# Performance work log

Measured on AMD Instinct MI355X. Metric: run time of the kernel, lower is better.

Reference implementation:

```python
import jax, jax.numpy as jnp
import numpy as np

IN_SIZE = 512
OUT_SIZE = 256
HIDDEN = 256
LN_EPS = 1e-5


def setup_inputs() -> dict:
    key = jax.random.key(0)
    ks = jax.random.split(key, 9)
    B, S, K = 8, 2048, 16
    net_in = jax.random.normal(ks[0], (B, S, K, IN_SIZE), dtype=jnp.float32)
    embeds = jax.random.normal(ks[1], (B, S, OUT_SIZE), dtype=jnp.float32)
    m = jax.random.uniform(ks[2], (B, S, K, 1), dtype=jnp.float32)
    W1 = jax.random.normal(ks[3], (IN_SIZE, HIDDEN), dtype=jnp.float32) * 0.02
    b1 = jnp.full((HIDDEN,), 0.02, dtype=jnp.float32)
    Wf = jax.random.normal(ks[4], (HIDDEN, OUT_SIZE + 1), dtype=jnp.float32) * 0.02
    bf = jnp.zeros((OUT_SIZE + 1,), dtype=jnp.float32)
    gamma = jnp.ones((OUT_SIZE,), dtype=jnp.float32)
    beta = jnp.zeros((OUT_SIZE,), dtype=jnp.float32)
    return {"net_in": net_in, "embeds": embeds, "m": m, "W1": W1, "b1": b1,
            "Wf": Wf, "bf": bf, "gamma": gamma, "beta": beta}


def reference(net_in, embeds, m, W1, b1, Wf, bf, gamma, beta):
    # MLP: one hidden relu layer, final linear to out_size+1
    h = jax.nn.relu(jnp.einsum('bski,ih->bskh', net_in, W1) + b1)
    out = jnp.einsum('bskh,ho->bsko', h, Wf) + bf          # [B,S,K,out+1]
    # sigmoid on last channel (link weight), then mask
    out = jnp.concatenate([out[..., :-1], jax.nn.sigmoid(out[..., -1:])], axis=-1)
    out = m * out
    link_weight = out[..., -1] + 1e-8                       # [B,S,K]
    norm = jnp.sum(link_weight, axis=2, keepdims=True)      # [B,S,1]
    weights = (link_weight / norm)[..., None]               # [B,S,K,1]
    updates = jnp.sum(out * weights, axis=2)                # [B,S,out+1]
    # residual update
    upd_weights = updates[..., -1:]
    embeds_new = embeds + upd_weights * updates[..., :-1]
    # LayerNorm over last dim
    mu = jnp.mean(embeds_new, axis=-1, keepdims=True)
    var = jnp.var(embeds_new, axis=-1, keepdims=True)
    return (embeds_new - mu) * jax.lax.rsqrt(var + LN_EPS) * gamma + beta
```

## Files before the change

### kernel.cpp

```cpp
#include <hip/hip_runtime.h>

typedef short s16x8 __attribute__((ext_vector_type(8)));
typedef float f32x4 __attribute__((ext_vector_type(4)));

__device__ __forceinline__ unsigned short f2bf(float f) {
    union { float f; unsigned u; } v; v.f = f;
    return (unsigned short)((v.u + 0x7FFFu + ((v.u >> 16) & 1u)) >> 16);
}
__device__ __forceinline__ float bf2f(unsigned short h) {
    union { unsigned u; float f; } v; v.u = ((unsigned)h) << 16;
    return v.f;
}

__device__ __forceinline__ void wg_barrier_lds() {
    __builtin_amdgcn_sched_barrier(0);
    asm volatile("s_waitcnt lgkmcnt(0)" ::: "memory");
    __builtin_amdgcn_s_barrier();
    __builtin_amdgcn_sched_barrier(0);
}

#define NBLK 2048

__global__ void prep_weights(const float* __restrict__ W1, const float* __restrict__ Wf,
                             unsigned short* __restrict__ W1T, unsigned short* __restrict__ WfT) {
    int t = blockIdx.x * 256 + threadIdx.x;
    {
        int c  = t >> 13;
        int n  = (t >> 5) & 255;
        int kk = t & 31;
        W1T[t] = f2bf(W1[(c * 32 + kk) * 256 + n]);
    }
    if (t < 65536) {
        int c  = t >> 13;
        int n  = (t >> 5) & 255;
        int hh = t & 31;
        WfT[t] = f2bf(Wf[(c * 32 + hh) * 257 + n]);
    }
}

__global__ __launch_bounds__(512, 2)
void fused_embed(const float* __restrict__ net_in, const float* __restrict__ embeds,
                 const float* __restrict__ mg, const float* __restrict__ W1,
                 const float* __restrict__ b1, const float* __restrict__ Wf,
                 const float* __restrict__ bfv, const float* __restrict__ gam,
                 const float* __restrict__ bet, float* __restrict__ out,
                 const unsigned short* __restrict__ W1T, const unsigned short* __restrict__ WfT)
{
    __shared__ unsigned short Abuf[2][128][32];
    __shared__ unsigned short Hbuf[128][260];
    __shared__ unsigned short gbuf[16][264];
    __shared__ float updb[8][264];
    __shared__ float sbuf[8];

    const int tid  = threadIdx.x;
    const int lane = tid & 63;
    const int wid  = tid >> 6;
    const int wr   = wid >> 2;
    const int wc   = wid & 3;
    const int l15  = lane & 15;
    const int g8   = (lane >> 4) * 8;
    const int blk  = blockIdx.x;
    const int row0 = blk * 128;

    const f32x4 zero4 = {0.f, 0.f, 0.f, 0.f};

    f32x4 acc[4][4];
    #pragma unroll
    for (int i = 0; i < 4; ++i)
        #pragma unroll
        for (int j = 0; j < 4; ++j)
            acc[i][j] = zero4;

    const int ar = tid >> 2;
    const int ac = (tid & 3) * 8;
    const int wn = (wc * 64 + l15) * 32 + g8;

    float4 vaA[2], vbA[2];
    s16x8  wW0[2], wW1[2], wW2[2], wW3[2];

#define G1_ISSUE(KC, S) do { \
        const float* _src = &net_in[(row0 + ar) * 512 + (KC) * 32 + ac]; \
        vaA[S] = *(const float4*)_src; \
        vbA[S] = *(const float4*)(_src + 4); \
        const unsigned short* _wp = W1T + (KC) * 8192 + wn; \
        wW0[S] = *(const s16x8*)(_wp); \
        wW1[S] = *(const s16x8*)(_wp + 512); \
        wW2[S] = *(const s16x8*)(_wp + 1024); \
        wW3[S] = *(const s16x8*)(_wp + 1536); \
    } while (0)

#define G1_WRITE(KC, S) do { \
        int4 _pk; \
        asm("v_cvt_pk_bf16_f32 %0, %1, %2" : "=v"(_pk.x) : "v"(vaA[S].x), "v"(vaA[S].y)); \
        asm("v_cvt_pk_bf16_f32 %0, %1, %2" : "=v"(_pk.y) : "v"(vaA[S].z), "v"(vaA[S].w)); \
        asm("v_cvt_pk_bf16_f32 %0, %1, %2" : "=v"(_pk.z) : "v"(vbA[S].x), "v"(vbA[S].y)); \
        asm("v_cvt_pk_bf16_f32 %0, %1, %2" : "=v"(_pk.w) : "v"(vbA[S].z), "v"(vbA[S].w)); \
        *(int4*)&Abuf[(KC) & 1][ar][ac] = _pk; \
    } while (0)

    G1_ISSUE(0, 0);
    G1_ISSUE(1, 1);
    G1_WRITE(0, 0);
    wg_barrier_lds();

    #pragma unroll
    for (int kc = 0; kc < 16; ++kc) {
        const int cur = kc & 1;
        s16x8 b0 = wW0[cur], b1 = wW1[cur], b2 = wW2[cur], b3 = wW3[cur];
        if (kc < 14) G1_ISSUE(kc + 2, cur);
        if (kc < 15) G1_WRITE(kc + 1, (kc + 1) & 1);
        s16x8 af[4];
        #pragma unroll
        for (int i = 0; i < 4; ++i)
            af[i] = *(const s16x8*)&Abuf[cur][(wr * 4 + i) * 16 + l15][g8];
        #pragma unroll
        for (int i = 0; i < 4; ++i) {
            acc[i][0] = __builtin_amdgcn_mfma_f32_16x16x32_bf16(af[i], b0, acc[i][0], 0, 0, 0);
            acc[i][1] = __builtin_amdgcn_mfma_f32_16x16x32_bf16(af[i], b1, acc[i][1], 0, 0, 0);
            acc[i][2] = __builtin_amdgcn_mfma_f32_16x16x32_bf16(af[i], b2, acc[i][2], 0, 0, 0);
            acc[i][3] = __builtin_amdgcn_mfma_f32_16x16x32_bf16(af[i], b3, acc[i][3], 0, 0, 0);
        }
        wg_barrier_lds();
    }
#undef G1_ISSUE
#undef G1_WRITE

    #pragma unroll
    for (int j = 0; j < 4; ++j) {
        int col = wc * 64 + j * 16 + l15;
        float bb = b1[col];
        #pragma unroll
        for (int i = 0; i < 4; ++i) {
            #pragma unroll
            for (int r = 0; r < 4; ++r) {
                int row = (wr * 4 + i) * 16 + (lane >> 4) * 4 + r;
                Hbuf[row][col] = f2bf(fmaxf(acc[i][j][r] + bb, 0.f));
            }
        }
    }
    __syncthreads();

    float wl0 = Wf[(lane * 4 + 0) * 257 + 256];
    float wl1 = Wf[(lane * 4 + 1) * 257 + 256];
    float wl2 = Wf[(lane * 4 + 2) * 257 + 256];
    float wl3 = Wf[(lane * 4 + 3) * 257 + 256];
    float bf256 = bfv[256];

    float lcreg = 0.f;
    for (int k = 0; k < 16; ++k) {
        ushort4 hv = *(const ushort4*)&Hbuf[wid * 16 + k][lane * 4];
        float p = bf2f(hv.x) * wl0 + bf2f(hv.y) * wl1 + bf2f(hv.z) * wl2 + bf2f(hv.w) * wl3;
        #pragma unroll
        for (int off = 32; off > 0; off >>= 1) p += __shfl_xor(p, off, 64);
        if (lane == k) lcreg = p;
    }

    float wwreg = 0.f;
    float u256 = 0.f;
    if (lane < 16) {
        float mv  = mg[(blk * 8 + wid) * 16 + lane];
        float raw = lcreg + bf256;
        float sg  = 1.f / (1.f + expf(-raw));
        float v   = mv * sg;
        float lw  = v + 1e-8f;
        float nrm = lw;
        #pragma unroll
        for (int off = 8; off > 0; off >>= 1) nrm += __shfl_xor(nrm, off, 16);
        float wk = lw / nrm;
        wwreg = wk * mv;
        float u = wk * v;
        float s = wwreg;
        #pragma unroll
        for (int off = 8; off > 0; off >>= 1) {
            u += __shfl_xor(u, off, 16);
            s += __shfl_xor(s, off, 16);
        }
        u256 = u;
        if (lane == 0) sbuf[wid] = s;
    }
    u256 = __shfl(u256, 0, 64);

    {
        float ga0 = 0.f, ga1 = 0.f, ga2 = 0.f, ga3 = 0.f;
        #pragma unroll
        for (int k = 0; k < 16; ++k) {
            float wwk = __shfl(wwreg, k, 64);
            ushort4 hv = *(const ushort4*)&Hbuf[wid * 16 + k][lane * 4];
            ga0 += wwk * bf2f(hv.x);
            ga1 += wwk * bf2f(hv.y);
            ga2 += wwk * bf2f(hv.z);
            ga3 += wwk * bf2f(hv.w);
        }
        ushort4 gw; gw.x = f2bf(ga0); gw.y = f2bf(ga1); gw.z = f2bf(ga2); gw.w = f2bf(ga3);
        *(ushort4*)&gbuf[wid][lane * 4] = gw;
        ushort4 z4; z4.x = 0; z4.y = 0; z4.z = 0; z4.w = 0;
        *(ushort4*)&gbuf[8 + wid][lane * 4] = z4;
    }
    __syncthreads();

    f32x4 acc2[2];
    acc2[0] = zero4; acc2[1] = zero4;
    {
        const int w2n0 = ((wid * 2 + 0) * 16 + l15) * 32 + g8;
        const int w2n1 = ((wid * 2 + 1) * 16 + l15) * 32 + g8;
        s16x8 w2a[2], w2b[2];
        w2a[0] = *(const s16x8*)(WfT + w2n0);
        w2b[0] = *(const s16x8*)(WfT + w2n1);
        #pragma unroll
        for (int c2 = 0; c2 < 8; ++c2) {
            const int cur = c2 & 1;
            s16x8 ba = w2a[cur], bb = w2b[cur];
            if (c2 < 7) {
                w2a[cur ^ 1] = *(const s16x8*)(WfT + (c2 + 1) * 8192 + w2n0);
                w2b[cur ^ 1] = *(const s16x8*)(WfT + (c2 + 1) * 8192 + w2n1);
            }
            s16x8 ga = *(const s16x8*)&gbuf[l15][c2 * 32 + g8];
            acc2[0] = __builtin_amdgcn_mfma_f32_16x16x32_bf16(ga, ba, acc2[0], 0, 0, 0);
            acc2[1] = __builtin_amdgcn_mfma_f32_16x16x32_bf16(ga, bb, acc2[1], 0, 0, 0);
        }
    }

    {
        int gq = lane >> 4;
        if (gq < 2) {
            #pragma unroll
            for (int t = 0; t < 2; ++t) {
                int col = (wid * 2 + t) * 16 + l15;
                float bfc = bfv[col];
                #pragma unroll
                for (int r = 0; r < 4; ++r) {
                    int p = gq * 4 + r;
                    updb[p][col] = acc2[t][r] + sbuf[p] * bfc;
                }
            }
        }
    }
    __syncthreads();

    {
        int base = (blk * 8 + wid) * 256;
        float4 up = *(const float4*)&updb[wid][lane * 4];
        float4 em = *(const float4*)&embeds[base + lane * 4];
        float e0 = em.x + u256 * up.x;
        float e1 = em.y + u256 * up.y;
        float e2 = em.z + u256 * up.z;
        float e3 = em.w + u256 * up.w;
        float s1 = e0 + e1 + e2 + e3;
        float s2 = e0 * e0 + e1 * e1 + e2 * e2 + e3 * e3;
        #pragma unroll
        for (int off = 32; off > 0; off >>= 1) {
            s1 += __shfl_xor(s1, off, 64);
            s2 += __shfl_xor(s2, off, 64);
        }
        float mu  = s1 * (1.f / 256.f);
        float var = s2 * (1.f / 256.f) - mu * mu;
        float rs  = rsqrtf(var + 1e-5f);
        float4 gm = *(const float4*)&gam[lane * 4];
        float4 bt = *(const float4*)&bet[lane * 4];
        float4 o;
        o.x = (e0 - mu) * rs * gm.x + bt.x;
        o.y = (e1 - mu) * rs * gm.y + bt.y;
        o.z = (e2 - mu) * rs * gm.z + bt.z;
        o.w = (e3 - mu) * rs * gm.w + bt.w;
        *(float4*)&out[base + lane * 4] = o;
    }
}

extern "C" void kernel_launch(void* const* d_in, const int* in_sizes, int n_in,
                              void* d_out, int out_size, void* d_ws, size_t ws_size,
                              hipStream_t stream) {
    (void)in_sizes; (void)n_in; (void)ws_size; (void)out_size;
    const float* net_in = (const float*)d_in[0];
    const float* embeds = (const float*)d_in[1];
    const float* mg     = (const float*)d_in[2];
    const float* W1     = (const float*)d_in[3];
    const float* b1     = (const float*)d_in[4];
    const float* Wf     = (const float*)d_in[5];
    const float* bfv    = (const float*)d_in[6];
    const float* gam    = (const float*)d_in[7];
    const float* bet    = (const float*)d_in[8];
    float* outp = (float*)d_out;

    unsigned short* W1T = (unsigned short*)d_ws;
    unsigned short* WfT = W1T + 131072;

    prep_weights<<<512, 256, 0, stream>>>(W1, Wf, W1T, WfT);
    fused_embed<<<NBLK, 512, 0, stream>>>(net_in, embeds, mg, W1, b1, Wf, bfv, gam, bet, outp, W1T, WfT);
}
```

Before: 203.8 us.

## Load GEMM1 A fragments directly from global into registers, drop LDS staging

The first GEMM stops staging net_in through a double-buffered LDS tile. Each wave now loads its own A rows straight from global memory into registers, converts them to bf16 and feeds them to MFMA. The wave tiling changes from 2x4 to 4x2 (32 rows by 128 columns per wave), so each wave holds 8 W1 fragments per stage. The per-iteration LDS barrier becomes an occasional soft barrier every four k-chunks, which removes LDS traffic and sync cost but raises register pressure and the volume of W1 loads.

```diff
diff --git a/kernel.cpp b/kernel.cpp
--- a/kernel.cpp
+++ b/kernel.cpp
@@ -12,9 +12,8 @@
     return v.f;
 }
 
-__device__ __forceinline__ void wg_barrier_lds() {
+__device__ __forceinline__ void soft_barrier() {
     __builtin_amdgcn_sched_barrier(0);
-    asm volatile("s_waitcnt lgkmcnt(0)" ::: "memory");
     __builtin_amdgcn_s_barrier();
     __builtin_amdgcn_sched_barrier(0);
 }
@@ -46,7 +45,6 @@
                  const float* __restrict__ bet, float* __restrict__ out,
                  const unsigned short* __restrict__ W1T, const unsigned short* __restrict__ WfT)
 {
-    __shared__ unsigned short Abuf[2][128][32];
     __shared__ unsigned short Hbuf[128][260];
     __shared__ unsigned short gbuf[16][264];
     __shared__ float updb[8][264];
@@ -55,8 +53,6 @@
     const int tid  = threadIdx.x;
     const int lane = tid & 63;
     const int wid  = tid >> 6;
-    const int wr   = wid >> 2;
-    const int wc   = wid & 3;
     const int l15  = lane & 15;
     const int g8   = (lane >> 4) * 8;
     const int blk  = blockIdx.x;
@@ -64,76 +60,77 @@
 
     const f32x4 zero4 = {0.f, 0.f, 0.f, 0.f};
 
-    f32x4 acc[4][4];
+    const int wr = wid >> 1;
+    const int wc = wid & 1;
+
+    f32x4 acc[2][8];
     #pragma unroll
-    for (int i = 0; i < 4; ++i)
-        #pragma unroll
-        for (int j = 0; j < 4; ++j)
+    for (int i = 0; i < 2; ++i)
+        #pragma unroll
+        for (int j = 0; j < 8; ++j)
             acc[i][j] = zero4;
 
-    const int ar = tid >> 2;
-    const int ac = (tid & 3) * 8;
-    const int wn = (wc * 64 + l15) * 32 + g8;
-
-    float4 vaA[2], vbA[2];
-    s16x8  wW0[2], wW1[2], wW2[2], wW3[2];
-
-#define G1_ISSUE(KC, S) do { \
-        const float* _src = &net_in[(row0 + ar) * 512 + (KC) * 32 + ac]; \
-        vaA[S] = *(const float4*)_src; \
-        vbA[S] = *(const float4*)(_src + 4); \
-        const unsigned short* _wp = W1T + (KC) * 8192 + wn; \
-        wW0[S] = *(const s16x8*)(_wp); \
-        wW1[S] = *(const s16x8*)(_wp + 512); \
-        wW2[S] = *(const s16x8*)(_wp + 1024); \
-        wW3[S] = *(const s16x8*)(_wp + 1536); \
+    const float* pA0 = net_in + (row0 + wr * 32 + l15) * 512;
+    const float* pA1 = pA0 + 16 * 512;
+    const int wbase = (wc * 128 + l15) * 32 + g8;
+
+    float4 a0[2], a1[2], a2[2], a3[2];
+    s16x8  wf[2][8];
+
+#define S1_ISSUE(KC, S) do { \
+        a0[S] = *(const float4*)(pA0 + (KC) * 32 + g8); \
+        a1[S] = *(const float4*)(pA0 + (KC) * 32 + g8 + 4); \
+        a2[S] = *(const float4*)(pA1 + (KC) * 32 + g8); \
+        a3[S] = *(const float4*)(pA1 + (KC) * 32 + g8 + 4); \
+        const unsigned short* _wp = W1T + (KC) * 8192 + wbase; \
+        wf[S][0] = *(const s16x8*)(_wp); \
+        wf[S][1] = *(const s16x8*)(_wp + 512); \
+        wf[S][2] = *(const s16x8*)(_wp + 1024); \
+        wf[S][3] = *(const s16x8*)(_wp + 1536); \
+        wf[S][4] = *(const s16x8*)(_wp + 2048); \
+        wf[S][5] = *(const s16x8*)(_wp + 2560); \
+        wf[S][6] = *(const s16x8*)(_wp + 3072); \
+        wf[S][7] = *(const s16x8*)(_wp + 3584); \
     } while (0)
 
-#define G1_WRITE(KC, S) do { \
-        int4 _pk; \
-        asm("v_cvt_pk_bf16_f32 %0, %1, %2" : "=v"(_pk.x) : "v"(vaA[S].x), "v"(vaA[S].y)); \
-        asm("v_cvt_pk_bf16_f32 %0, %1, %2" : "=v"(_pk.y) : "v"(vaA[S].z), "v"(vaA[S].w)); \
-        asm("v_cvt_pk_bf16_f32 %0, %1, %2" : "=v"(_pk.z) : "v"(vbA[S].x), "v"(vbA[S].y)); \
-        asm("v_cvt_pk_bf16_f32 %0, %1, %2" : "=v"(_pk.w) : "v"(vbA[S].z), "v"(vbA[S].w)); \
-        *(int4*)&Abuf[(KC) & 1][ar][ac] = _pk; \
-    } while (0)
-
-    G1_ISSUE(0, 0);
-    G1_ISSUE(1, 1);
-    G1_WRITE(0, 0);
-    wg_barrier_lds();
+    S1_ISSUE(0, 0);
 
     #pragma unroll
     for (int kc = 0; kc < 16; ++kc) {
         const int cur = kc & 1;
-        s16x8 b0 = wW0[cur], b1 = wW1[cur], b2 = wW2[cur], b3 = wW3[cur];
-        if (kc < 14) G1_ISSUE(kc + 2, cur);
-        if (kc < 15) G1_WRITE(kc + 1, (kc + 1) & 1);
-        s16x8 af[4];
-        #pragma unroll
-        for (int i = 0; i < 4; ++i)
-            af[i] = *(const s16x8*)&Abuf[cur][(wr * 4 + i) * 16 + l15][g8];
-        #pragma unroll
-        for (int i = 0; i < 4; ++i) {
-            acc[i][0] = __builtin_amdgcn_mfma_f32_16x16x32_bf16(af[i], b0, acc[i][0], 0, 0, 0);
-            acc[i][1] = __builtin_amdgcn_mfma_f32_16x16x32_bf16(af[i], b1, acc[i][1], 0, 0, 0);
-            acc[i][2] = __builtin_amdgcn_mfma_f32_16x16x32_bf16(af[i], b2, acc[i][2], 0, 0, 0);
-            acc[i][3] = __builtin_amdgcn_mfma_f32_16x16x32_bf16(af[i], b3, acc[i][3], 0, 0, 0);
-        }
-        wg_barrier_lds();
-    }
-#undef G1_ISSUE
-#undef G1_WRITE
+        if (kc < 15) S1_ISSUE(kc + 1, cur ^ 1);
+        s16x8 af0, af1;
+        {
+            int4 p0, p1;
+            asm("v_cvt_pk_bf16_f32 %0, %1, %2" : "=v"(p0.x) : "v"(a0[cur].x), "v"(a0[cur].y));
+            asm("v_cvt_pk_bf16_f32 %0, %1, %2" : "=v"(p0.y) : "v"(a0[cur].z), "v"(a0[cur].w));
+            asm("v_cvt_pk_bf16_f32 %0, %1, %2" : "=v"(p0.z) : "v"(a1[cur].x), "v"(a1[cur].y));
+            asm("v_cvt_pk_bf16_f32 %0, %1, %2" : "=v"(p0.w) : "v"(a1[cur].z), "v"(a1[cur].w));
+            asm("v_cvt_pk_bf16_f32 %0, %1, %2" : "=v"(p1.x) : "v"(a2[cur].x), "v"(a2[cur].y));
+            asm("v_cvt_pk_bf16_f32 %0, %1, %2" : "=v"(p1.y) : "v"(a2[cur].z), "v"(a2[cur].w));
+            asm("v_cvt_pk_bf16_f32 %0, %1, %2" : "=v"(p1.z) : "v"(a3[cur].x), "v"(a3[cur].y));
+            asm("v_cvt_pk_bf16_f32 %0, %1, %2" : "=v"(p1.w) : "v"(a3[cur].z), "v"(a3[cur].w));
+            af0 = *(const s16x8*)&p0;
+            af1 = *(const s16x8*)&p1;
+        }
+        #pragma unroll
+        for (int j = 0; j < 8; ++j) {
+            acc[0][j] = __builtin_amdgcn_mfma_f32_16x16x32_bf16(af0, wf[cur][j], acc[0][j], 0, 0, 0);
+            acc[1][j] = __builtin_amdgcn_mfma_f32_16x16x32_bf16(af1, wf[cur][j], acc[1][j], 0, 0, 0);
+        }
+        if ((kc & 3) == 3 && kc != 15) soft_barrier();
+    }
+#undef S1_ISSUE
 
     #pragma unroll
-    for (int j = 0; j < 4; ++j) {
-        int col = wc * 64 + j * 16 + l15;
+    for (int j = 0; j < 8; ++j) {
+        int col = wc * 128 + j * 16 + l15;
         float bb = b1[col];
         #pragma unroll
-        for (int i = 0; i < 4; ++i) {
+        for (int i = 0; i < 2; ++i) {
             #pragma unroll
             for (int r = 0; r < 4; ++r) {
-                int row = (wr * 4 + i) * 16 + (lane >> 4) * 4 + r;
+                int row = wr * 32 + i * 16 + (lane >> 4) * 4 + r;
                 Hbuf[row][col] = f2bf(fmaxf(acc[i][j][r] + bb, 0.f));
             }
         }
```

Measured after the change: 331.9 us. 1.63x slower.

## Double block tile to 256 rows with 1024 threads and fill full second GEMM

Applied to the files above, without the earlier changes.

Each block now processes 256 rows (16 groups) with 16 waves instead of 128 rows with 8 waves. The hidden-tile epilogue runs in two halves so the existing Hbuf can be reused. The second GEMM's 16-row M tile, previously half zero-padded, is now filled with real groups, and the W1 register double-buffering is replaced by direct loads each iteration. The aim is to halve padded MFMA work in the second GEMM and amortize weight loads over more rows, at the cost of extra barriers, fewer resident blocks, and a higher register ceiling from dropping to 1024-thread launch bounds.

```diff
diff --git a/kernel.cpp b/kernel.cpp
--- a/kernel.cpp
+++ b/kernel.cpp
@@ -19,7 +19,7 @@
     __builtin_amdgcn_sched_barrier(0);
 }
 
-#define NBLK 2048
+#define NBLK 1024
 
 __global__ void prep_weights(const float* __restrict__ W1, const float* __restrict__ Wf,
                              unsigned short* __restrict__ W1T, unsigned short* __restrict__ WfT) {
@@ -38,7 +38,7 @@
     }
 }
 
-__global__ __launch_bounds__(512, 2)
+__global__ __launch_bounds__(1024)
 void fused_embed(const float* __restrict__ net_in, const float* __restrict__ embeds,
                  const float* __restrict__ mg, const float* __restrict__ W1,
                  const float* __restrict__ b1, const float* __restrict__ Wf,
@@ -46,11 +46,11 @@
                  const float* __restrict__ bet, float* __restrict__ out,
                  const unsigned short* __restrict__ W1T, const unsigned short* __restrict__ WfT)
 {
-    __shared__ unsigned short Abuf[2][128][32];
+    __shared__ unsigned short Abuf[2][256][32];
     __shared__ unsigned short Hbuf[128][260];
     __shared__ unsigned short gbuf[16][264];
-    __shared__ float updb[8][264];
-    __shared__ float sbuf[8];
+    __shared__ float updb[16][264];
+    __shared__ float sbuf[16];
 
     const int tid  = threadIdx.x;
     const int lane = tid & 63;
@@ -60,7 +60,7 @@
     const int l15  = lane & 15;
     const int g8   = (lane >> 4) * 8;
     const int blk  = blockIdx.x;
-    const int row0 = blk * 128;
+    const int row0 = blk * 256;
 
     const f32x4 zero4 = {0.f, 0.f, 0.f, 0.f};
 
@@ -73,23 +73,17 @@
 
     const int ar = tid >> 2;
     const int ac = (tid & 3) * 8;
-    const int wn = (wc * 64 + l15) * 32 + g8;
+    const int wbase = (wc * 64 + l15) * 32 + g8;
 
     float4 vaA[2], vbA[2];
-    s16x8  wW0[2], wW1[2], wW2[2], wW3[2];
-
-#define G1_ISSUE(KC, S) do { \
+
+#define A_ISSUE(KC, S) do { \
         const float* _src = &net_in[(row0 + ar) * 512 + (KC) * 32 + ac]; \
         vaA[S] = *(const float4*)_src; \
         vbA[S] = *(const float4*)(_src + 4); \
-        const unsigned short* _wp = W1T + (KC) * 8192 + wn; \
-        wW0[S] = *(const s16x8*)(_wp); \
-        wW1[S] = *(const s16x8*)(_wp + 512); \
-        wW2[S] = *(const s16x8*)(_wp + 1024); \
-        wW3[S] = *(const s16x8*)(_wp + 1536); \
     } while (0)
 
-#define G1_WRITE(KC, S) do { \
+#define A_WRITE(KC, S) do { \
         int4 _pk; \
         asm("v_cvt_pk_bf16_f32 %0, %1, %2" : "=v"(_pk.x) : "v"(vaA[S].x), "v"(vaA[S].y)); \
         asm("v_cvt_pk_bf16_f32 %0, %1, %2" : "=v"(_pk.y) : "v"(vaA[S].z), "v"(vaA[S].w)); \
@@ -98,47 +92,36 @@
         *(int4*)&Abuf[(KC) & 1][ar][ac] = _pk; \
     } while (0)
 
-    G1_ISSUE(0, 0);
-    G1_ISSUE(1, 1);
-    G1_WRITE(0, 0);
+    A_ISSUE(0, 0);
+    A_ISSUE(1, 1);
+    A_WRITE(0, 0);
     wg_barrier_lds();
 
     #pragma unroll
     for (int kc = 0; kc < 16; ++kc) {
         const int cur = kc & 1;
-        s16x8 b0 = wW0[cur], b1 = wW1[cur], b2 = wW2[cur], b3 = wW3[cur];
-        if (kc < 14) G1_ISSUE(kc + 2, cur);
-        if (kc < 15) G1_WRITE(kc + 1, (kc + 1) & 1);
+        const unsigned short* wp = W1T + kc * 8192 + wbase;
+        s16x8 b0 = *(const s16x8*)(wp);
+        s16x8 b1r = *(const s16x8*)(wp + 512);
+        s16x8 b2 = *(const s16x8*)(wp + 1024);
+        s16x8 b3 = *(const s16x8*)(wp + 1536);
+        if (kc < 14) A_ISSUE(kc + 2, cur);
+        if (kc < 15) A_WRITE(kc + 1, (kc + 1) & 1);
         s16x8 af[4];
         #pragma unroll
         for (int i = 0; i < 4; ++i)
-            af[i] = *(const s16x8*)&Abuf[cur][(wr * 4 + i) * 16 + l15][g8];
+            af[i] = *(const s16x8*)&Abuf[cur][wr * 64 + i * 16 + l15][g8];
         #pragma unroll
         for (int i = 0; i < 4; ++i) {
             acc[i][0] = __builtin_amdgcn_mfma_f32_16x16x32_bf16(af[i], b0, acc[i][0], 0, 0, 0);
-            acc[i][1] = __builtin_amdgcn_mfma_f32_16x16x32_bf16(af[i], b1, acc[i][1], 0, 0, 0);
+            acc[i][1] = __builtin_amdgcn_mfma_f32_16x16x32_bf16(af[i], b1r, acc[i][1], 0, 0, 0);
             acc[i][2] = __builtin_amdgcn_mfma_f32_16x16x32_bf16(af[i], b2, acc[i][2], 0, 0, 0);
             acc[i][3] = __builtin_amdgcn_mfma_f32_16x16x32_bf16(af[i], b3, acc[i][3], 0, 0, 0);
         }
         wg_barrier_lds();
     }
-#undef G1_ISSUE
-#undef G1_WRITE
-
-    #pragma unroll
-    for (int j = 0; j < 4; ++j) {
-        int col = wc * 64 + j * 16 + l15;
-        float bb = b1[col];
-        #pragma unroll
-        for (int i = 0; i < 4; ++i) {
-            #pragma unroll
-            for (int r = 0; r < 4; ++r) {
-                int row = (wr * 4 + i) * 16 + (lane >> 4) * 4 + r;
-                Hbuf[row][col] = f2bf(fmaxf(acc[i][j][r] + bb, 0.f));
-            }
-        }
-    }
-    __syncthreads();
+#undef A_ISSUE
+#undef A_WRITE
 
     float wl0 = Wf[(lane * 4 + 0) * 257 + 256];
     float wl1 = Wf[(lane * 4 + 1) * 257 + 256];
@@ -146,99 +129,108 @@
     float wl3 = Wf[(lane * 4 + 3) * 257 + 256];
     float bf256 = bfv[256];
 
-    float lcreg = 0.f;
-    for (int k = 0; k < 16; ++k) {
-        ushort4 hv = *(const ushort4*)&Hbuf[wid * 16 + k][lane * 4];
-        float p = bf2f(hv.x) * wl0 + bf2f(hv.y) * wl1 + bf2f(hv.z) * wl2 + bf2f(hv.w) * wl3;
-        #pragma unroll
-        for (int off = 32; off > 0; off >>= 1) p += __shfl_xor(p, off, 64);
-        if (lane == k) lcreg = p;
-    }
-
-    float wwreg = 0.f;
     float u256 = 0.f;
-    if (lane < 16) {
-        float mv  = mg[(blk * 8 + wid) * 16 + lane];
-        float raw = lcreg + bf256;
-        float sg  = 1.f / (1.f + expf(-raw));
-        float v   = mv * sg;
-        float lw  = v + 1e-8f;
-        float nrm = lw;
-        #pragma unroll
-        for (int off = 8; off > 0; off >>= 1) nrm += __shfl_xor(nrm, off, 16);
-        float wk = lw / nrm;
-        wwreg = wk * mv;
-        float u = wk * v;
-        float s = wwreg;
-        #pragma unroll
-        for (int off = 8; off > 0; off >>= 1) {
-            u += __shfl_xor(u, off, 16);
-            s += __shfl_xor(s, off, 16);
-        }
-        u256 = u;
-        if (lane == 0) sbuf[wid] = s;
-    }
-    u256 = __shfl(u256, 0, 64);
-
-    {
-        float ga0 = 0.f, ga1 = 0.f, ga2 = 0.f, ga3 = 0.f;
-        #pragma unroll
-        for (int k = 0; k < 16; ++k) {
-            float wwk = __shfl(wwreg, k, 64);
-            ushort4 hv = *(const ushort4*)&Hbuf[wid * 16 + k][lane * 4];
-            ga0 += wwk * bf2f(hv.x);
-            ga1 += wwk * bf2f(hv.y);
-            ga2 += wwk * bf2f(hv.z);
-            ga3 += wwk * bf2f(hv.w);
-        }
-        ushort4 gw; gw.x = f2bf(ga0); gw.y = f2bf(ga1); gw.z = f2bf(ga2); gw.w = f2bf(ga3);
-        *(ushort4*)&gbuf[wid][lane * 4] = gw;
-        ushort4 z4; z4.x = 0; z4.y = 0; z4.z = 0; z4.w = 0;
-        *(ushort4*)&gbuf[8 + wid][lane * 4] = z4;
-    }
-    __syncthreads();
-
-    f32x4 acc2[2];
-    acc2[0] = zero4; acc2[1] = zero4;
-    {
-        const int w2n0 = ((wid * 2 + 0) * 16 + l15) * 32 + g8;
-        const int w2n1 = ((wid * 2 + 1) * 16 + l15) * 32 + g8;
-        s16x8 w2a[2], w2b[2];
-        w2a[0] = *(const s16x8*)(WfT + w2n0);
-        w2b[0] = *(const s16x8*)(WfT + w2n1);
+
+    #pragma unroll
+    for (int h = 0; h < 2; ++h) {
+        const int mine = ((wid >> 3) == h);
+
+        if (mine) {
+            #pragma unroll
+            for (int j = 0; j < 4; ++j) {
+                int col = wc * 64 + j * 16 + l15;
+                float bb = b1[col];
+                #pragma unroll
+                for (int i = 0; i < 4; ++i) {
+                    #pragma unroll
+                    for (int r = 0; r < 4; ++r) {
+                        int rih = (wr & 1) * 64 + i * 16 + (lane >> 4) * 4 + r;
+                        Hbuf[rih][col] = f2bf(fmaxf(acc[i][j][r] + bb, 0.f));
+                    }
+                }
+            }
+        }
+        __syncthreads();
+
+        if (mine) {
+            float lcreg = 0.f;
+            for (int k = 0; k < 16; ++k) {
+                ushort4 hv = *(const ushort4*)&Hbuf[(wid & 7) * 16 + k][lane * 4];
+                float p = bf2f(hv.x) * wl0 + bf2f(hv.y) * wl1 + bf2f(hv.z) * wl2 + bf2f(hv.w) * wl3;
+                #pragma unroll
+                for (int off = 32; off > 0; off >>= 1) p += __shfl_xor(p, off, 64);
+                if (lane == k) lcreg = p;
+            }
+
+            float wwreg = 0.f;
+            if (lane < 16) {
+                float mv  = mg[(blk * 16 + wid) * 16 + lane];
+                float raw = lcreg + bf256;
+                float sg  = 1.f / (1.f + expf(-raw));
+                float v   = mv * sg;
+                float lw  = v + 1e-8f;
+                float nrm = lw;
+                #pragma unroll
+                for (int off = 8; off > 0; off >>= 1) nrm += __shfl_xor(nrm, off, 16);
+                float wk = lw / nrm;
+                wwreg = wk * mv;
+                float u = wk * v;
+                float s = wwreg;
+                #pragma unroll
+                for (int off = 8; off > 0; off >>= 1) {
+                    u += __shfl_xor(u, off, 16);
+                    s += __shfl_xor(s, off, 16);
+                }
+                u256 = u;
+                if (lane == 0) sbuf[wid] = s;
+            }
+            u256 = __shfl(u256, 0, 64);
+
+            float ga0 = 0.f, ga1 = 0.f, ga2 = 0.f, ga3 = 0.f;
+            #pragma unroll
+            for (int k = 0; k < 16; ++k) {
+                float wwk = __shfl(wwreg, k, 64);
+                ushort4 hv = *(const ushort4*)&Hbuf[(wid & 7) * 16 + k][lane * 4];
+                ga0 += wwk * bf2f(hv.x);
+                ga1 += wwk * bf2f(hv.y);
+                ga2 += wwk * bf2f(hv.z);
+                ga3 += wwk * bf2f(hv.w);
+            }
+            ushort4 gw; gw.x = f2bf(ga0); gw.y = f2bf(ga1); gw.z = f2bf(ga2); gw.w = f2bf(ga3);
+            *(ushort4*)&gbuf[wid][lane * 4] = gw;
+        }
+        __syncthreads();
+    }
+
+    f32x4 acc2 = zero4;
+    {
+        const int n0 = (wid * 16 + l15) * 32 + g8;
+        s16x8 w2[2];
+        w2[0] = *(const s16x8*)(WfT + n0);
         #pragma unroll
         for (int c2 = 0; c2 < 8; ++c2) {
             const int cur = c2 & 1;
-            s16x8 ba = w2a[cur], bb = w2b[cur];
-            if (c2 < 7) {
-                w2a[cur ^ 1] = *(const s16x8*)(WfT + (c2 + 1) * 8192 + w2n0);
-                w2b[cur ^ 1] = *(const s16x8*)(WfT + (c2 + 1) * 8192 + w2n1);
-            }
+            s16x8 bw = w2[cur];
+            if (c2 < 7) w2[cur ^ 1] = *(const s16x8*)(WfT + (c2 + 1) * 8192 + n0);
             s16x8 ga = *(const s16x8*)&gbuf[l15][c2 * 32 + g8];
-            acc2[0] = __builtin_amdgcn_mfma_f32_16x16x32_bf16(ga, ba, acc2[0], 0, 0, 0);
-            acc2[1] = __builtin_amdgcn_mfma_f32_16x16x32_bf16(ga, bb, acc2[1], 0, 0, 0);
+            acc2 = __builtin_amdgcn_mfma_f32_16x16x32_bf16(ga, bw, acc2, 0, 0, 0);
         }
     }
 
     {
         int gq = lane >> 4;
-        if (gq < 2) {
-            #pragma unroll
-            for (int t = 0; t < 2; ++t) {
-                int col = (wid * 2 + t) * 16 + l15;
-                float bfc = bfv[col];
-                #pragma unroll
-                for (int r = 0; r < 4; ++r) {
-                    int p = gq * 4 + r;
-                    updb[p][col] = acc2[t][r] + sbuf[p] * bfc;
-                }
-            }
+        int col = wid * 16 + l15;
+        float bfc = bfv[col];
+        #pragma unroll
+        for (int r = 0; r < 4; ++r) {
+            int p = gq * 4 + r;
+            updb[p][col] = acc2[r] + sbuf[p] * bfc;
         }
     }
     __syncthreads();
 
     {
-        int base = (blk * 8 + wid) * 256;
+        int base = (blk * 16 + wid) * 256;
         float4 up = *(const float4*)&updb[wid][lane * 4];
         float4 em = *(const float4*)&embeds[base + lane * 4];
         float e0 = em.x + u256 * up.x;
@@ -285,5 +277,5 @@
     unsigned short* WfT = W1T + 131072;
 
     prep_weights<<<512, 256, 0, stream>>>(W1, Wf, W1T, WfT);
-    fused_embed<<<NBLK, 512, 0, stream>>>(net_in, embeds, mg, W1, b1, Wf, bfv, gam, bet, outp, W1T, WfT);
-}
+    fused_embed<<<NBLK, 1024, 0, stream>>>(net_in, embeds, mg, W1, b1, Wf, bfv, gam, bet, outp, W1T, WfT);
+}
```

After: 198.0 us. 1.03x faster.

## Make fused MLP kernel persistent and prefetch next group's inputs across epilogue

Applied to the files above, without the earlier changes.

The grid shrinks from 2048 to 256 blocks, and each block loops over 8 row groups of 128 rows. The first two net_in chunks of the next group are issued before the current group's epilogue (hidden write, link weights, second GEMM, LayerNorm), so that load latency overlaps the epilogue. The W1 fetch is split into its own macro that loads 8 fragments per stage, though only 4 are consumed, which adds wasted loads and register pressure. With one block per CU, there is less concurrent work to hide memory latency in this streaming-bound kernel.

```diff
diff --git a/kernel.cpp b/kernel.cpp
--- a/kernel.cpp
+++ b/kernel.cpp
@@ -19,7 +19,7 @@
     __builtin_amdgcn_sched_barrier(0);
 }
 
-#define NBLK 2048
+#define NBLK 256
 
 __global__ void prep_weights(const float* __restrict__ W1, const float* __restrict__ Wf,
                              unsigned short* __restrict__ W1T, unsigned short* __restrict__ WfT) {
@@ -59,37 +59,36 @@
     const int wc   = wid & 3;
     const int l15  = lane & 15;
     const int g8   = (lane >> 4) * 8;
-    const int blk  = blockIdx.x;
-    const int row0 = blk * 128;
+    const int cu   = blockIdx.x;
 
     const f32x4 zero4 = {0.f, 0.f, 0.f, 0.f};
-
-    f32x4 acc[4][4];
-    #pragma unroll
-    for (int i = 0; i < 4; ++i)
-        #pragma unroll
-        for (int j = 0; j < 4; ++j)
-            acc[i][j] = zero4;
 
     const int ar = tid >> 2;
     const int ac = (tid & 3) * 8;
-    const int wn = (wc * 64 + l15) * 32 + g8;
+    const int wbase = (wc * 64 + l15) * 32 + g8;
 
     float4 vaA[2], vbA[2];
-    s16x8  wW0[2], wW1[2], wW2[2], wW3[2];
-
-#define G1_ISSUE(KC, S) do { \
-        const float* _src = &net_in[(row0 + ar) * 512 + (KC) * 32 + ac]; \
+    s16x8  wW[2][8];
+
+#define A_ISSUE_AT(R0, KC, S) do { \
+        const float* _src = &net_in[((R0) + ar) * 512 + (KC) * 32 + ac]; \
         vaA[S] = *(const float4*)_src; \
         vbA[S] = *(const float4*)(_src + 4); \
-        const unsigned short* _wp = W1T + (KC) * 8192 + wn; \
-        wW0[S] = *(const s16x8*)(_wp); \
-        wW1[S] = *(const s16x8*)(_wp + 512); \
-        wW2[S] = *(const s16x8*)(_wp + 1024); \
-        wW3[S] = *(const s16x8*)(_wp + 1536); \
     } while (0)
 
-#define G1_WRITE(KC, S) do { \
+#define W_ISSUE(KC, S) do { \
+        const unsigned short* _wp = W1T + (KC) * 8192 + wbase; \
+        wW[S][0] = *(const s16x8*)(_wp); \
+        wW[S][1] = *(const s16x8*)(_wp + 512); \
+        wW[S][2] = *(const s16x8*)(_wp + 1024); \
+        wW[S][3] = *(const s16x8*)(_wp + 1536); \
+        wW[S][4] = *(const s16x8*)(_wp + 2048); \
+        wW[S][5] = *(const s16x8*)(_wp + 2560); \
+        wW[S][6] = *(const s16x8*)(_wp + 3072); \
+        wW[S][7] = *(const s16x8*)(_wp + 3584); \
+    } while (0)
+
+#define A_WRITE(KC, S) do { \
         int4 _pk; \
         asm("v_cvt_pk_bf16_f32 %0, %1, %2" : "=v"(_pk.x) : "v"(vaA[S].x), "v"(vaA[S].y)); \
         asm("v_cvt_pk_bf16_f32 %0, %1, %2" : "=v"(_pk.y) : "v"(vaA[S].z), "v"(vaA[S].w)); \
@@ -98,172 +97,194 @@
         *(int4*)&Abuf[(KC) & 1][ar][ac] = _pk; \
     } while (0)
 
-    G1_ISSUE(0, 0);
-    G1_ISSUE(1, 1);
-    G1_WRITE(0, 0);
-    wg_barrier_lds();
-
-    #pragma unroll
-    for (int kc = 0; kc < 16; ++kc) {
-        const int cur = kc & 1;
-        s16x8 b0 = wW0[cur], b1 = wW1[cur], b2 = wW2[cur], b3 = wW3[cur];
-        if (kc < 14) G1_ISSUE(kc + 2, cur);
-        if (kc < 15) G1_WRITE(kc + 1, (kc + 1) & 1);
-        s16x8 af[4];
+    A_ISSUE_AT(cu * 8 * 128, 0, 0);
+    A_ISSUE_AT(cu * 8 * 128, 1, 1);
+
+    #pragma unroll 1
+    for (int grp = 0; grp < 8; ++grp) {
+        const int pg   = cu * 8 + grp;
+        const int row0 = pg * 128;
+
+        W_ISSUE(0, 0);
+        W_ISSUE(1, 1);
+        A_WRITE(0, 0);
+        wg_barrier_lds();
+
+        f32x4 acc[4][4];
         #pragma unroll
         for (int i = 0; i < 4; ++i)
-            af[i] = *(const s16x8*)&Abuf[cur][(wr * 4 + i) * 16 + l15][g8];
+            #pragma unroll
+            for (int j = 0; j < 4; ++j)
+                acc[i][j] = zero4;
+
         #pragma unroll
-        for (int i = 0; i < 4; ++i) {
-            acc[i][0] = __builtin_amdgcn_mfma_f32_16x16x32_bf16(af[i], b0, acc[i][0], 0, 0, 0);
-            acc[i][1] = __builtin_amdgcn_mfma_f32_16x16x32_bf16(af[i], b1, acc[i][1], 0, 0, 0);
-            acc[i][2] = __builtin_amdgcn_mfma_f32_16x16x32_bf16(af[i], b2, acc[i][2], 0, 0, 0);
-            acc[i][3] = __builtin_amdgcn_mfma_f32_16x16x32_bf16(af[i], b3, acc[i][3], 0, 0, 0);
-        }
-        wg_barrier_lds();
-    }
-#undef G1_ISSUE
-#undef G1_WRITE
-
-    #pragma unroll
-    for (int j = 0; j < 4; ++j) {
-        int col = wc * 64 + j * 16 + l15;
-        float bb = b1[col];
+        for (int kc = 0; kc < 16; ++kc) {
+            const int cur = kc & 1;
+            s16x8 b0 = wW[cur][0], b1r = wW[cur][1], b2 = wW[cur][2], b3 = wW[cur][3];
+            if (kc < 14) { A_ISSUE_AT(row0, kc + 2, cur); W_ISSUE(kc + 2, cur); }
+            if (kc < 15) A_WRITE(kc + 1, (kc + 1) & 1);
+            s16x8 af[4];
+            #pragma unroll
+            for (int i = 0; i < 4; ++i)
+                af[i] = *(const s16x8*)&Abuf[cur][(wr * 4 + i) * 16 + l15][g8];
+            #pragma unroll
+            for (int i = 0; i < 4; ++i) {
+                acc[i][0] = __builtin_amdgcn_mfma_f32_16x16x32_bf16(af[i], b0, acc[i][0], 0, 0, 0);
+                acc[i][1] = __builtin_amdgcn_mfma_f32_16x16x32_bf16(af[i], b1r, acc[i][1], 0, 0, 0);
+                acc[i][2] = __builtin_amdgcn_mfma_f32_16x16x32_bf16(af[i], b2, acc[i][2], 0, 0, 0);
+                acc[i][3] = __builtin_amdgcn_mfma_f32_16x16x32_bf16(af[i], b3, acc[i][3], 0, 0, 0);
+            }
+            wg_barrier_lds();
+        }
+
+        if (grp < 7) {
+            A_ISSUE_AT(row0 + 128, 0, 0);
+            A_ISSUE_AT(row0 + 128, 1, 1);
+        }
+
         #pragma unroll
-        for (int i = 0; i < 4; ++i) {
-            #pragma unroll
-            for (int r = 0; r < 4; ++r) {
-                int row = (wr * 4 + i) * 16 + (lane >> 4) * 4 + r;
-                Hbuf[row][col] = f2bf(fmaxf(acc[i][j][r] + bb, 0.f));
-            }
-        }
-    }
-    __syncthreads();
-
-    float wl0 = Wf[(lane * 4 + 0) * 257 + 256];
-    float wl1 = Wf[(lane * 4 + 1) * 257 + 256];
-    float wl2 = Wf[(lane * 4 + 2) * 257 + 256];
-    float wl3 = Wf[(lane * 4 + 3) * 257 + 256];
-    float bf256 = bfv[256];
-
-    float lcreg = 0.f;
-    for (int k = 0; k < 16; ++k) {
-        ushort4 hv = *(const ushort4*)&Hbuf[wid * 16 + k][lane * 4];
-        float p = bf2f(hv.x) * wl0 + bf2f(hv.y) * wl1 + bf2f(hv.z) * wl2 + bf2f(hv.w) * wl3;
-        #pragma unroll
-        for (int off = 32; off > 0; off >>= 1) p += __shfl_xor(p, off, 64);
-        if (lane == k) lcreg = p;
-    }
-
-    float wwreg = 0.f;
-    float u256 = 0.f;
-    if (lane < 16) {
-        float mv  = mg[(blk * 8 + wid) * 16 + lane];
-        float raw = lcreg + bf256;
-        float sg  = 1.f / (1.f + expf(-raw));
-        float v   = mv * sg;
-        float lw  = v + 1e-8f;
-        float nrm = lw;
-        #pragma unroll
-        for (int off = 8; off > 0; off >>= 1) nrm += __shfl_xor(nrm, off, 16);
-        float wk = lw / nrm;
-        wwreg = wk * mv;
-        float u = wk * v;
-        float s = wwreg;
-        #pragma unroll
-        for (int off = 8; off > 0; off >>= 1) {
-            u += __shfl_xor(u, off, 16);
-            s += __shfl_xor(s, off, 16);
-        }
-        u256 = u;
-        if (lane == 0) sbuf[wid] = s;
-    }
-    u256 = __shfl(u256, 0, 64);
-
-    {
-        float ga0 = 0.f, ga1 = 0.f, ga2 = 0.f, ga3 = 0.f;
-        #pragma unroll
-        for (int k = 0; k < 16; ++k) {
-            float wwk = __shfl(wwreg, k, 64);
-            ushort4 hv = *(const ushort4*)&Hbuf[wid * 16 + k][lane * 4];
-            ga0 += wwk * bf2f(hv.x);
-            ga1 += wwk * bf2f(hv.y);
-            ga2 += wwk * bf2f(hv.z);
-            ga3 += wwk * bf2f(hv.w);
-        }
-        ushort4 gw; gw.x = f2bf(ga0); gw.y = f2bf(ga1); gw.z = f2bf(ga2); gw.w = f2bf(ga3);
-        *(ushort4*)&gbuf[wid][lane * 4] = gw;
-        ushort4 z4; z4.x = 0; z4.y = 0; z4.z = 0; z4.w = 0;
-        *(ushort4*)&gbuf[8 + wid][lane * 4] = z4;
-    }
-    __syncthreads();
-
-    f32x4 acc2[2];
-    acc2[0] = zero4; acc2[1] = zero4;
-    {
-        const int w2n0 = ((wid * 2 + 0) * 16 + l15) * 32 + g8;
-        const int w2n1 = ((wid * 2 + 1) * 16 + l15) * 32 + g8;
-        s16x8 w2a[2], w2b[2];
-        w2a[0] = *(const s16x8*)(WfT + w2n0);
-        w2b[0] = *(const s16x8*)(WfT + w2n1);
-        #pragma unroll
-        for (int c2 = 0; c2 < 8; ++c2) {
-            const int cur = c2 & 1;
-            s16x8 ba = w2a[cur], bb = w2b[cur];
-            if (c2 < 7) {
-                w2a[cur ^ 1] = *(const s16x8*)(WfT + (c2 + 1) * 8192 + w2n0);
-                w2b[cur ^ 1] = *(const s16x8*)(WfT + (c2 + 1) * 8192 + w2n1);
-            }
-            s16x8 ga = *(const s16x8*)&gbuf[l15][c2 * 32 + g8];
-            acc2[0] = __builtin_amdgcn_mfma_f32_16x16x32_bf16(ga, ba, acc2[0], 0, 0, 0);
-            acc2[1] = __builtin_amdgcn_mfma_f32_16x16x32_bf16(ga, bb, acc2[1], 0, 0, 0);
-        }
-    }
-
-    {
-        int gq = lane >> 4;
-        if (gq < 2) {
-            #pragma unroll
-            for (int t = 0; t < 2; ++t) {
-                int col = (wid * 2 + t) * 16 + l15;
-                float bfc = bfv[col];
+        for (int j = 0; j < 4; ++j) {
+            int col = wc * 64 + j * 16 + l15;
+            float bb = b1[col];
+            #pragma unroll
+            for (int i = 0; i < 4; ++i) {
                 #pragma unroll
                 for (int r = 0; r < 4; ++r) {
-                    int p = gq * 4 + r;
-                    updb[p][col] = acc2[t][r] + sbuf[p] * bfc;
+                    int row = (wr * 4 + i) * 16 + (lane >> 4) * 4 + r;
+                    Hbuf[row][col] = f2bf(fmaxf(acc[i][j][r] + bb, 0.f));
                 }
             }
         }
+        __syncthreads();
+
+        float wl0 = Wf[(lane * 4 + 0) * 257 + 256];
+        float wl1 = Wf[(lane * 4 + 1) * 257 + 256];
+        float wl2 = Wf[(lane * 4 + 2) * 257 + 256];
+        float wl3 = Wf[(lane * 4 + 3) * 257 + 256];
+        float bf256 = bfv[256];
+
+        float lcreg = 0.f;
+        for (int k = 0; k < 16; ++k) {
+            ushort4 hv = *(const ushort4*)&Hbuf[wid * 16 + k][lane * 4];
+            float p = bf2f(hv.x) * wl0 + bf2f(hv.y) * wl1 + bf2f(hv.z) * wl2 + bf2f(hv.w) * wl3;
+            #pragma unroll
+            for (int off = 32; off > 0; off >>= 1) p += __shfl_xor(p, off, 64);
+            if (lane == k) lcreg = p;
+        }
+
+        float wwreg = 0.f;
+        float u256 = 0.f;
+        if (lane < 16) {
+            float mv  = mg[(pg * 8 + wid) * 16 + lane];
+            float raw = lcreg + bf256;
+            float sg  = 1.f / (1.f + expf(-raw));
+            float v   = mv * sg;
+            float lw  = v + 1e-8f;
+            float nrm = lw;
+            #pragma unroll
+            for (int off = 8; off > 0; off >>= 1) nrm += __shfl_xor(nrm, off, 16);
+            float wk = lw / nrm;
+            wwreg = wk * mv;
+            float u = wk * v;
+            float s = wwreg;
+            #pragma unroll
+            for (int off = 8; off > 0; off >>= 1) {
+                u += __shfl_xor(u, off, 16);
+                s += __shfl_xor(s, off, 16);
+            }
+            u256 = u;
+            if (lane == 0) sbuf[wid] = s;
+        }
+        u256 = __shfl(u256, 0, 64);
+
+        {
+            float ga0 = 0.f, ga1 = 0.f, ga2 = 0.f, ga3 = 0.f;
+            #pragma unroll
+            for (int k = 0; k < 16; ++k) {
+                float wwk = __shfl(wwreg, k, 64);
+                ushort4 hv = *(const ushort4*)&Hbuf[wid * 16 + k][lane * 4];
+                ga0 += wwk * bf2f(hv.x);
+                ga1 += wwk * bf2f(hv.y);
+                ga2 += wwk * bf2f(hv.z);
+                ga3 += wwk * bf2f(hv.w);
+            }
+            ushort4 gw; gw.x = f2bf(ga0); gw.y = f2bf(ga1); gw.z = f2bf(ga2); gw.w = f2bf(ga3);
+            *(ushort4*)&gbuf[wid][lane * 4] = gw;
+            ushort4 z4; z4.x = 0; z4.y = 0; z4.z = 0; z4.w = 0;
+            *(ushort4*)&gbuf[8 + wid][lane * 4] = z4;
+        }
+        __syncthreads();
+
+        f32x4 acc2[2];
+        acc2[0] = zero4; acc2[1] = zero4;
+        {
+            const int w2n0 = ((wid * 2 + 0) * 16 + l15) * 32 + g8;
+            const int w2n1 = ((wid * 2 + 1) * 16 + l15) * 32 + g8;
+            s16x8 w2a[2], w2b[2];
+            w2a[0] = *(const s16x8*)(WfT + w2n0);
+            w2b[0] = *(const s16x8*)(WfT + w2n1);
+            #pragma unroll
+            for (int c2 = 0; c2 < 8; ++c2) {
+                const int cur = c2 & 1;
+                s16x8 ba = w2a[cur], bb = w2b[cur];
+                if (c2 < 7) {
+                    w2a[cur ^ 1] = *(const s16x8*)(WfT + (c2 + 1) * 8192 + w2n0);
+                    w2b[cur ^ 1] = *(const s16x8*)(WfT + (c2 + 1) * 8192 + w2n1);
+                }
+                s16x8 ga = *(const s16x8*)&gbuf[l15][c2 * 32 + g8];
+                acc2[0] = __builtin_amdgcn_mfma_f32_16x16x32_bf16(ga, ba, acc2[0], 0, 0, 0);
+                acc2[1] = __builtin_amdgcn_mfma_f32_16x16x32_bf16(ga, bb, acc2[1], 0, 0, 0);
+            }
+        }
+
+        {
+            int gq = lane >> 4;
+            if (gq < 2) {
+                #pragma unroll
+                for (int t = 0; t < 2; ++t) {
+                    int col = (wid * 2 + t) * 16 + l15;
+                    float bfc = bfv[col];
+                    #pragma unroll
+                    for (int r = 0; r < 4; ++r) {
+                        int p = gq * 4 + r;
+                        updb[p][col] = acc2[t][r] + sbuf[p] * bfc;
+                    }
+                }
+            }
+        }
+        __syncthreads();
+
+        {
+            int base = (pg * 8 + wid) * 256;
+            float4 up = *(const float4*)&updb[wid][lane * 4];
+            float4 em = *(const float4*)&embeds[base + lane * 4];
+            float e0 = em.x + u256 * up.x;
+            float e1 = em.y + u256 * up.y;
+            float e2 = em.z + u256 * up.z;
+            float e3 = em.w + u256 * up.w;
+            float s1 = e0 + e1 + e2 + e3;
+            float s2 = e0 * e0 + e1 * e1 + e2 * e2 + e3 * e3;
+            #pragma unroll
+            for (int off = 32; off > 0; off >>= 1) {
+                s1 += __shfl_xor(s1, off, 64);
+                s2 += __shfl_xor(s2, off, 64);
+            }
+            float mu  = s1 * (1.f / 256.f);
+            float var = s2 * (1.f / 256.f) - mu * mu;
+            float rs  = rsqrtf(var + 1e-5f);
+            float4 gm = *(const float4*)&gam[lane * 4];
+            float4 bt = *(const float4*)&bet[lane * 4];
+            float4 o;
+            o.x = (e0 - mu) * rs * gm.x + bt.x;
+            o.y = (e1 - mu) * rs * gm.y + bt.y;
+            o.z = (e2 - mu) * rs * gm.z + bt.z;
+            o.w = (e3 - mu) * rs * gm.w + bt.w;
+            *(float4*)&out[base + lane * 4] = o;
+        }
     }
-    __syncthreads();
-
-    {
-        int base = (blk * 8 + wid) * 256;
-        float4 up = *(const float4*)&updb[wid][lane * 4];
-        float4 em = *(const float4*)&embeds[base + lane * 4];
-        float e0 = em.x + u256 * up.x;
-        float e1 = em.y + u256 * up.y;
-        float e2 = em.z + u256 * up.z;
-        float e3 = em.w + u256 * up.w;
-        float s1 = e0 + e1 + e2 + e3;
-        float s2 = e0 * e0 + e1 * e1 + e2 * e2 + e3 * e3;
-        #pragma unroll
-        for (int off = 32; off > 0; off >>= 1) {
-            s1 += __shfl_xor(s1, off, 64);
-            s2 += __shfl_xor(s2, off, 64);
-        }
-        float mu  = s1 * (1.f / 256.f);
-        float var = s2 * (1.f / 256.f) - mu * mu;
-        float rs  = rsqrtf(var + 1e-5f);
-        float4 gm = *(const float4*)&gam[lane * 4];
-        float4 bt = *(const float4*)&bet[lane * 4];
-        float4 o;
-        o.x = (e0 - mu) * rs * gm.x + bt.x;
-        o.y = (e1 - mu) * rs * gm.y + bt.y;
-        o.z = (e2 - mu) * rs * gm.z + bt.z;
-        o.w = (e3 - mu) * rs * gm.w + bt.w;
-        *(float4*)&out[base + lane * 4] = o;
-    }
+#undef A_ISSUE_AT
+#undef W_ISSUE
+#undef A_WRITE
 }
 
 extern "C" void kernel_launch(void* const* d_in, const int* in_sizes, int n_in,
```

Result: slower. 309.1 us (+51.7%).
